# Kernel tuning notes

Hardware: AMD Instinct MI355X
Metric: run time of the kernel (lower is better)

## Reference

```python
import jax, jax.numpy as jnp
import numpy as np

B, NPB, K = 8, 4096, 16            # batches, points per batch, knn neighbors
IN_FEAT, OUT_FEAT, N_HEADS = 64, 64, 8
N = B * NPB
HD = OUT_FEAT // N_HEADS           # per-head dim (linear_w output width)
EPS = 1e-5


def _bn(x, g, b):
    # LayerNorm1d == BatchNorm1d over channel dim with stats across (N, k)
    m = jnp.mean(x, axis=(0, 1), keepdims=True)
    v = jnp.mean((x - m) ** 2, axis=(0, 1), keepdims=True)
    return (x - m) * jax.lax.rsqrt(v + EPS) * g + b


def _knn_idx(feat):
    # per-batch self-KNN in feature space (torch_geometric.nn.knn(x, x, k, batch, batch))
    f = feat.reshape(B, NPB, -1)
    sq = jnp.sum(f * f, axis=-1)                               # [B, n]
    d = sq[:, :, None] + sq[:, None, :] - 2.0 * jnp.einsum('bnc,bmc->bnm', f, f)
    _, idx = jax.lax.top_k(-d, K)                              # [B, n, K]
    idx = idx + (jnp.arange(B) * NPB)[:, None, None]           # global indices
    return idx.reshape(N, K)


def setup_inputs() -> dict:
    key = jax.random.key(0)
    ks = jax.random.split(key, 12)
    s = 0.05
    return {
        "p": jax.random.normal(ks[0], (N, 3), dtype=jnp.float32),
        "x": jax.random.normal(ks[1], (N, IN_FEAT), dtype=jnp.float32),
        "o": jnp.full((B,), NPB, dtype=jnp.int32),
        # q/k/v projections
        "wq": jax.random.normal(ks[2], (IN_FEAT, OUT_FEAT)) * s, "bq": jnp.zeros((OUT_FEAT,)),
        "wk": jax.random.normal(ks[3], (IN_FEAT, OUT_FEAT)) * s, "bk": jnp.zeros((OUT_FEAT,)),
        "wv": jax.random.normal(ks[4], (IN_FEAT, OUT_FEAT)) * s, "bv": jnp.zeros((OUT_FEAT,)),
        # linear_p: Linear(3,3) -> BN(3) -> ReLU -> Linear(3, out)
        "wp1": jax.random.normal(ks[5], (3, 3)) * s, "bp1": jnp.zeros((3,)),
        "gp": jnp.ones((3,)), "btp": jnp.zeros((3,)),
        "wp2": jax.random.normal(ks[6], (3, OUT_FEAT)) * s, "bp2": jnp.zeros((OUT_FEAT,)),
        # linear_w: BN(mid) -> ReLU -> Linear(mid, hd) -> BN(hd) -> ReLU -> Linear(hd, hd)
        "g1": jnp.ones((OUT_FEAT,)), "bt1": jnp.zeros((OUT_FEAT,)),
        "ww1": jax.random.normal(ks[7], (OUT_FEAT, HD)) * s, "bw1": jnp.zeros((HD,)),
        "g2": jnp.ones((HD,)), "bt2": jnp.zeros((HD,)),
        "ww2": jax.random.normal(ks[8], (HD, HD)) * s, "bw2": jnp.zeros((HD,)),
    }


def reference(p, x, o, wq, bq, wk, bk, wv, bv, wp1, bp1, gp, btp, wp2, bp2,
              g1, bt1, ww1, bw1, g2, bt2, ww2, bw2):
    # o encodes equal-size batches (NPB each); structure is baked into the knn helper.
    xq = x @ wq + bq                      # [N, mid]
    xk = x @ wk + bk                      # [N, mid]
    xv = x @ wv + bv                      # [N, out]
    idx_k = _knn_idx(xk)                  # KNN in k-feature space
    idx_v = _knn_idx(xv)                  # separate KNN in v-feature space (as in source)
    xk_g = xk[idx_k]                      # [N, K, mid]
    p_rel = p[idx_k] - p[:, None, :]      # grouped relative xyz [N, K, 3]
    xv_g = xv[idx_v]                      # [N, K, out]
    # position encoding MLP
    h = p_rel @ wp1 + bp1
    h = jax.nn.relu(_bn(h, gp, btp))
    p_r = h @ wp2 + bp2                   # [N, K, out]; einops.reduce with i=1 is identity
    # relation features and attention-weight MLP
    r = xk_g - xq[:, None, :] + p_r       # [N, K, mid]
    w = jax.nn.relu(_bn(r, g1, bt1)) @ ww1 + bw1
    w = jax.nn.relu(_bn(w, g2, bt2)) @ ww2 + bw2   # [N, K, HD]
    w = jax.nn.softmax(w, axis=1)         # softmax over neighbors
    comb = (xv_g + p_r).reshape(N, K, N_HEADS, HD)
    out = jnp.einsum('ntsi,nti->nsi', comb, w).reshape(N, OUT_FEAT)
    return out
```

## Files before the change

kernel.cpp:

```cpp
#include <hip/hip_runtime.h>
#include <hip/hip_bf16.h>

typedef __hip_bfloat16 bf16;

#define NPTS  32768
#define NPB   4096
#define NPAIR (NPTS*16)
#define IMASK 32767
#define EPSB  1e-5f

#define O_WQ  0
#define O_BQ  4096
#define O_WK  4160
#define O_BK  8256
#define O_WV  8320
#define O_BV  12416
#define O_WP1 12480
#define O_BP1 12489
#define O_GP  12492
#define O_BTP 12495
#define O_WP2 12498
#define O_BP2 12690
#define O_G1  12754
#define O_BT1 12818
#define O_WW1 12882
#define O_BW1 13394
#define O_G2  13402
#define O_BT2 13410
#define O_WW2 13418
#define O_BW2 13482
#define NPRM  13490

__device__ __forceinline__ float b2f(bf16 v){ return __bfloat162float(v); }
__device__ __forceinline__ float u16f(unsigned short u){ return __uint_as_float(((unsigned)u)<<16); }
__device__ __forceinline__ float ldany(const void* p, long long i, int f32){
    return f32 ? ((const float*)p)[i] : b2f(((const bf16*)p)[i]);
}

__device__ __forceinline__ void split2(float x, unsigned &h, unsigned &m){
    unsigned u  = __float_as_uint(x);
    unsigned hr = (u + 0x7FFFu + ((u>>16)&1u)) & 0xFFFF0000u;
    float xm = x - __uint_as_float(hr);
    h = hr >> 16;
    m = __float_as_uint(xm) >> 16;
}

__global__ __launch_bounds__(256) void k_sniff(const void* x, const void* wq, int* flags)
{
    __shared__ float red[2][4];
    const unsigned short* xu = (const unsigned short*)x;
    const unsigned short* wu = (const unsigned short*)wq;
    const int tid = threadIdx.x, lane = tid & 63, wvi = tid >> 6;
    float mx = fabsf(u16f(xu[tid]));
    float mw = fabsf(u16f(wu[tid]));
    for (int off = 32; off; off >>= 1){
        mx = fmaxf(mx, __shfl_down(mx, off));
        mw = fmaxf(mw, __shfl_down(mw, off));
    }
    if (lane == 0){ red[0][wvi] = mx; red[1][wvi] = mw; }
    __syncthreads();
    if (tid == 0){
        float ax = fmaxf(fmaxf(red[0][0], red[0][1]), fmaxf(red[0][2], red[0][3]));
        float aw = fmaxf(fmaxf(red[1][0], red[1][1]), fmaxf(red[1][2], red[1][3]));
        flags[0] = (ax > 1e6f) ? 1 : 0;
        flags[1] = (aw > 1e6f) ? 1 : 0;
    }
}

struct P20 { const void* p[20]; };

__global__ __launch_bounds__(256) void k_conv(P20 t, const void* __restrict__ p,
                                              const int* __restrict__ flags,
                                              float* __restrict__ prm, float* __restrict__ p32)
{
    const int i = blockIdx.x*256 + threadIdx.x;
    if (i < NPRM){
        const int f = flags[1];
        const int sz[20] = {4096,64,4096,64,4096,64,9,3,3,3,192,64,64,64,512,8,8,8,64,8};
        int seg = 0, rem = i;
        while (rem >= sz[seg]){ rem -= sz[seg]; ++seg; }
        prm[i] = ldany(t.p[seg], rem, f);
    } else {
        const int j = i - NPRM;
        if (j < NPTS*3) p32[j] = ldany(p, j, flags[0]);
    }
}

__global__ __launch_bounds__(256) void k_proj(
    const void* __restrict__ x, const int* __restrict__ flags,
    const float* __restrict__ prm,
    float* __restrict__ xq, float* __restrict__ xk, float* __restrict__ xv,
    float* __restrict__ sqk, float* __restrict__ sqv,
    unsigned* __restrict__ hkp, unsigned* __restrict__ mkp,
    unsigned* __restrict__ hvp, unsigned* __restrict__ mvp)
{
    __shared__ float WQ[4096], WK[4096], WV[4096], BQ[64], BK[64], BV[64];
    const int tid = threadIdx.x;
    for (int i = tid; i < 4096; i += 256){
        WQ[i] = prm[O_WQ+i]; WK[i] = prm[O_WK+i]; WV[i] = prm[O_WV+i];
    }
    if (tid < 64){ BQ[tid]=prm[O_BQ+tid]; BK[tid]=prm[O_BK+tid]; BV[tid]=prm[O_BV+tid]; }
    const int f32 = flags[0];
    __syncthreads();
    const int lane = tid & 63, wvi = tid >> 6;
    const int ptbase = blockIdx.x*16 + wvi*4;
    for (int it = 0; it < 4; ++it){
        const int pt = ptbase + it;
        float xl = ldany(x, (long long)pt*64 + lane, f32);
        float aq = BQ[lane], ak = BK[lane], av = BV[lane];
        #pragma unroll
        for (int k = 0; k < 64; ++k){
            float xb = __shfl(xl, k);
            aq += xb*WQ[k*64+lane];
            ak += xb*WK[k*64+lane];
            av += xb*WV[k*64+lane];
        }
        xq[pt*64+lane]=aq; xk[pt*64+lane]=ak; xv[pt*64+lane]=av;
        unsigned hk16, mk16, hv16, mv16;
        split2(ak, hk16, mk16); split2(av, hv16, mv16);
        unsigned hkn = __shfl_down(hk16,1), mkn = __shfl_down(mk16,1);
        unsigned hvn = __shfl_down(hv16,1), mvn = __shfl_down(mv16,1);
        if (!(lane & 1)){
            const int u = lane >> 3, pos = u ^ (pt & 7);
            const size_t gi = (size_t)pt*32 + pos*4 + ((lane & 7) >> 1);
            hkp[gi] = hk16 | (hkn<<16);  mkp[gi] = mk16 | (mkn<<16);
            hvp[gi] = hv16 | (hvn<<16);  mvp[gi] = mv16 | (mvn<<16);
        }
        float s1 = ak*ak, s2 = av*av;
        for (int off=32; off; off>>=1){ s1 += __shfl_down(s1,off); s2 += __shfl_down(s2,off); }
        if (lane==0){ sqk[pt]=s1; sqv[pt]=s2; }
    }
}


using bfrag  = __attribute__((ext_vector_type(8))) short;
using f32x4v = __attribute__((ext_vector_type(4))) float;

__device__ __forceinline__ int lds_sw(int row, int unit){
    return (row<<6) + (((unit ^ row) & 7)<<3);
}

__global__ __launch_bounds__(256, 4) void k_knn_part(
    const float* __restrict__ featk, const float* __restrict__ featv,
    const unsigned* __restrict__ hkp, const unsigned* __restrict__ mkp,
    const unsigned* __restrict__ hvp, const unsigned* __restrict__ mvp,
    const float* __restrict__ sqk, const float* __restrict__ sqv,
    const float* __restrict__ p32, const float* __restrict__ prm,
    int* __restrict__ idx_k, int* __restrict__ idx_v,
    float* __restrict__ part1)
{
    __shared__ __attribute__((aligned(16))) unsigned char smem[34048];
    __shared__ float bn1red[4][6];
    unsigned short* Ch = (unsigned short*)smem;
    unsigned short* Cm = (unsigned short*)(smem + 8192);
    float* Dt  = (float*)(smem + 16384);
    float* sqC = (float*)(smem + 16384 + 17408);
    unsigned long long* Lbuf = (unsigned long long*)smem;

    const int tid = threadIdx.x;
    const int swz = ((int)blockIdx.x & 7) * 128 + ((int)blockIdx.x >> 3);
    const int kid = swz >> 9;
    const int bid = swz & 511;
    const float*    feat = kid ? featv : featk;
    const float*    sq   = kid ? sqv  : sqk;
    const unsigned* hpl  = kid ? hvp : hkp;
    const unsigned* mpl  = kid ? mvp : mkp;
    const int b  = bid >> 6;
    const int qt = bid & 63;
    const int q0 = b*NPB + qt*64;
    const int cb = b*NPB;

    const int lane = tid & 63, wv = tid >> 6;
    const int lq = lane & 15, lg = lane >> 4;
    const int selq = (wv << 4) + (lane >> 2);
    const int sub  = lane & 3;
    const int owner = lane & ~3;
    const int row1 = tid >> 3, pos1 = tid & 7;
    const int row2 = row1 + 32;

    bfrag qh[2], qm[2];
    {
        const int qr = q0 + (wv<<4) + lq;
        #pragma unroll
        for (int ks = 0; ks < 2; ++ks){
            const int u0 = ks*4 + lg;
            const int pos = u0 ^ (qr & 7);
            union { uint4 u; bfrag v; } ch, cm;
            ch.u = *(const uint4*)&hpl[(size_t)qr*32 + pos*4];
            cm.u = *(const uint4*)&mpl[(size_t)qr*32 + pos*4];
            qh[ks] = ch.v; qm[ks] = cm.v;
        }
    }

    float d5[5]; int i5[5];
    #pragma unroll
    for (int i=0;i<5;++i){ d5[i] = 3.4e38f; i5[i] = 0; }

    const unsigned* hrow1 = hpl + (size_t)cb*32 + (size_t)row1*32 + pos1*4;
    const unsigned* hrow2 = hpl + (size_t)cb*32 + (size_t)row2*32 + pos1*4;
    const unsigned* mrow1 = mpl + (size_t)cb*32 + (size_t)row1*32 + pos1*4;
    const unsigned* mrow2 = mpl + (size_t)cb*32 + (size_t)row2*32 + pos1*4;
    const int ldsoff1 = row1*64 + pos1*8, ldsoff2 = row2*64 + pos1*8;

    {
        uint4 a1 = *(const uint4*)hrow1; uint4 a2 = *(const uint4*)hrow2;
        uint4 b1 = *(const uint4*)mrow1; uint4 b2 = *(const uint4*)mrow2;
        *(uint4*)&Ch[ldsoff1] = a1; *(uint4*)&Ch[ldsoff2] = a2;
        *(uint4*)&Cm[ldsoff1] = b1; *(uint4*)&Cm[ldsoff2] = b2;
        if (tid < 64) sqC[tid] = sq[cb + tid];
    }
    __syncthreads();

    #define MFMA_PHASE() { \
        _Pragma("unroll") \
        for (int ct = 0; ct < 4; ++ct){ \
            const int cd = ct*16 + lq; \
            union { uint4 u; bfrag v; } bh0u, bh1u, bm0u, bm1u; \
            bh0u.u = *(const uint4*)&Ch[lds_sw(cd, lg)]; \
            bh1u.u = *(const uint4*)&Ch[lds_sw(cd, 4+lg)]; \
            bm0u.u = *(const uint4*)&Cm[lds_sw(cd, lg)]; \
            bm1u.u = *(const uint4*)&Cm[lds_sw(cd, 4+lg)]; \
            f32x4v a = {0.f, 0.f, 0.f, 0.f}; \
            a = __builtin_amdgcn_mfma_f32_16x16x32_bf16(qm[0], bm0u.v, a, 0, 0, 0); \
            a = __builtin_amdgcn_mfma_f32_16x16x32_bf16(qm[1], bm1u.v, a, 0, 0, 0); \
            a = __builtin_amdgcn_mfma_f32_16x16x32_bf16(qh[0], bm0u.v, a, 0, 0, 0); \
            a = __builtin_amdgcn_mfma_f32_16x16x32_bf16(qm[0], bh0u.v, a, 0, 0, 0); \
            a = __builtin_amdgcn_mfma_f32_16x16x32_bf16(qh[1], bm1u.v, a, 0, 0, 0); \
            a = __builtin_amdgcn_mfma_f32_16x16x32_bf16(qm[1], bh1u.v, a, 0, 0, 0); \
            a = __builtin_amdgcn_mfma_f32_16x16x32_bf16(qh[0], bh0u.v, a, 0, 0, 0); \
            a = __builtin_amdgcn_mfma_f32_16x16x32_bf16(qh[1], bh1u.v, a, 0, 0, 0); \
            const float sc = sqC[ct*16 + lq]; \
            _Pragma("unroll") \
            for (int r = 0; r < 4; ++r) \
                Dt[((wv<<4) + (lg<<2) + r)*68 + ct*16 + lq] = sc - 2.f*a[r]; \
        } }

    MFMA_PHASE()

    for (int chn = 0; chn < 64; ++chn){
        __syncthreads();
        const bool more = (chn+1 < 64);
        uint4 a1, a2, b1, b2; float sqr = 0.f;
        if (more){
            const size_t co = (size_t)(chn+1)*2048;
            a1 = *(const uint4*)(hrow1 + co); a2 = *(const uint4*)(hrow2 + co);
            b1 = *(const uint4*)(mrow1 + co); b2 = *(const uint4*)(mrow2 + co);
            if (tid < 64) sqr = sq[cb + (chn+1)*64 + tid];
        }
        {
            float worst = __shfl(d5[4], owner+3);
            unsigned m16 = 0;
            const int rowoff = selq*68 + sub*16;
            #pragma unroll
            for (int r = 0; r < 4; ++r){
                float4 v = *(const float4*)&Dt[rowoff + 4*r];
                m16 |= (v.x < worst ? 1u : 0u) << (4*r+0);
                m16 |= (v.y < worst ? 1u : 0u) << (4*r+1);
                m16 |= (v.z < worst ? 1u : 0u) << (4*r+2);
                m16 |= (v.w < worst ? 1u : 0u) << (4*r+3);
            }
            unsigned ma = __shfl(m16, owner+0), mb = __shfl(m16, owner+1);
            unsigned mc = __shfl(m16, owner+2), md = __shfl(m16, owner+3);
            unsigned long long m = (unsigned long long)ma
                                 | ((unsigned long long)mb << 16)
                                 | ((unsigned long long)mc << 32)
                                 | ((unsigned long long)md << 48);
            const int qrow = selq*68;
            const int c0 = cb + chn*64;
            const int prevlane = (lane - 1) & 63;
            while (m){
                int c = (int)__builtin_ctzll(m); m &= m - 1;
                float d = Dt[qrow + c];
                int gi = c0 + c;
                float pl = __shfl(d5[4], prevlane);
                int   pi = __shfl(i5[4], prevlane);
                bool takePrev = (sub != 0) && (pl > d);
                float v  = takePrev ? pl : d;
                int   vi = takePrev ? pi : gi;
                #pragma unroll
                for (int i = 4; i >= 1; --i){
                    bool sh   = d5[i-1] > v;
                    bool here = !sh && (d5[i] > v);
                    d5[i] = sh ? d5[i-1] : (here ? v  : d5[i]);
                    i5[i] = sh ? i5[i-1] : (here ? vi : i5[i]);
                }
                bool h0 = d5[0] > v;
                d5[0] = h0 ? v  : d5[0];
                i5[0] = h0 ? vi : i5[0];
            }
        }
        if (more){
            *(uint4*)&Ch[ldsoff1] = a1; *(uint4*)&Ch[ldsoff2] = a2;
            *(uint4*)&Cm[ldsoff1] = b1; *(uint4*)&Cm[ldsoff2] = b2;
            if (tid < 64) sqC[tid] = sqr;
        }
        __syncthreads();
        if (more) MFMA_PHASE()
    }
    #undef MFMA_PHASE

    unsigned long long k5[5];
    {
        const float* qrow = feat + (size_t)(q0 + selq)*64;
        #pragma unroll
        for (int s = 0; s < 5; ++s){
            const int gi = i5[s];
            const float* crow = feat + (size_t)gi*64;
            float acc = 0.f;
            #pragma unroll
            for (int k4 = 0; k4 < 16; ++k4){
                float4 qv = *(const float4*)&qrow[4*k4];
                float4 cv = *(const float4*)&crow[4*k4];
                acc += qv.x*cv.x; acc += qv.y*cv.y; acc += qv.z*cv.z; acc += qv.w*cv.w;
            }
            float d = sq[gi] - 2.f*acc;
            unsigned ud = __float_as_uint(d);
            ud ^= (ud & 0x80000000u) ? 0xFFFFFFFFu : 0x80000000u;
            k5[s] = ((unsigned long long)ud << 32) | (unsigned)gi;
        }
    }
    #pragma unroll
    for (int pass = 0; pass < 5; ++pass){
        #pragma unroll
        for (int i = (pass & 1); i + 1 < 5; i += 2){
            unsigned long long a = k5[i], bb = k5[i+1];
            bool sw = a > bb;
            k5[i]   = sw ? bb : a;
            k5[i+1] = sw ? a : bb;
        }
    }
    __syncthreads();
    #pragma unroll
    for (int j = 0; j < 5; ++j) Lbuf[(size_t)tid*6 + j] = k5[j];
    Lbuf[(size_t)tid*6 + 5] = ~0ull;
    __syncthreads();
    int fi[16];
    #pragma unroll
    for (int i = 0; i < 16; ++i) fi[i] = 0;
    if (sub == 0){
        const unsigned long long* L0 = &Lbuf[(size_t)(tid+0)*6];
        const unsigned long long* L1 = &Lbuf[(size_t)(tid+1)*6];
        const unsigned long long* L2 = &Lbuf[(size_t)(tid+2)*6];
        const unsigned long long* L3 = &Lbuf[(size_t)(tid+3)*6];
        int p0 = 0, p1 = 0, p2 = 0, p3 = 0;
        #pragma unroll
        for (int o = 0; o < 16; ++o){
            unsigned long long b0 = L0[p0], b1v = L1[p1], b2v = L2[p2], b3v = L3[p3];
            unsigned long long m01 = (b0  < b1v) ? b0  : b1v;  int s01 = (b0  < b1v) ? 0 : 1;
            unsigned long long m23 = (b2v < b3v) ? b2v : b3v;  int s23 = (b2v < b3v) ? 2 : 3;
            unsigned long long mm  = (m01 < m23) ? m01 : m23;  int ss  = (m01 < m23) ? s01 : s23;
            fi[o] = (int)(unsigned)(mm & 0xFFFFFFFFull);
            if      (ss == 0) ++p0;
            else if (ss == 1) ++p1;
            else if (ss == 2) ++p2;
            else              ++p3;
        }
        int* idx_out = kid ? idx_v : idx_k;
        #pragma unroll
        for (int i4 = 0; i4 < 4; ++i4)
            *(int4*)&idx_out[(size_t)(q0+selq)*16 + 4*i4] =
                make_int4(fi[4*i4], fi[4*i4+1], fi[4*i4+2], fi[4*i4+3]);
    }

    if (kid == 0){
        const float w00=prm[O_WP1+0], w01=prm[O_WP1+1], w02=prm[O_WP1+2];
        const float w10=prm[O_WP1+3], w11=prm[O_WP1+4], w12=prm[O_WP1+5];
        const float w20=prm[O_WP1+6], w21=prm[O_WP1+7], w22=prm[O_WP1+8];
        const float bb0=prm[O_BP1+0], bb1=prm[O_BP1+1], bb2=prm[O_BP1+2];
        const size_t gq = (size_t)(q0 + selq);
        const float px=p32[gq*3+0], py=p32[gq*3+1], pz=p32[gq*3+2];
        float s0=0.f,s1=0.f,s2=0.f,t0=0.f,t1=0.f,t2=0.f;
        #pragma unroll
        for (int o = 0; o < 16; ++o){
            int gi = __shfl(fi[o], owner);
            if ((o & 3) == sub){
                const int j = gi & IMASK;
                float rx = p32[j*3+0]-px, ry = p32[j*3+1]-py, rz = p32[j*3+2]-pz;
                float h0 = bb0 + rx*w00 + ry*w10 + rz*w20;
                float h1 = bb1 + rx*w01 + ry*w11 + rz*w21;
                float h2 = bb2 + rx*w02 + ry*w12 + rz*w22;
                s0+=h0; s1+=h1; s2+=h2; t0+=h0*h0; t1+=h1*h1; t2+=h2*h2;
            }
        }
        #pragma unroll
        for (int off = 1; off < 64; off <<= 1){
            s0+=__shfl_down(s0,off); s1+=__shfl_down(s1,off); s2+=__shfl_down(s2,off);
            t0+=__shfl_down(t0,off); t1+=__shfl_down(t1,off); t2+=__shfl_down(t2,off);
        }
        if (lane == 0){
            bn1red[wv][0]=s0; bn1red[wv][1]=s1; bn1red[wv][2]=s2;
            bn1red[wv][3]=t0; bn1red[wv][4]=t1; bn1red[wv][5]=t2;
        }
        __syncthreads();
        if (tid < 6)
            part1[(size_t)tid*512 + bid] =
                bn1red[0][tid]+bn1red[1][tid]+bn1red[2][tid]+bn1red[3][tid];
    }
}

__global__ __launch_bounds__(256) void k_bnred_par(
    const float* __restrict__ part, int G, int C,
    const float* __restrict__ gamma, const float* __restrict__ beta,
    float* __restrict__ aff, float invCount)
{
    __shared__ float rs[4], rq[4];
    const int c = blockIdx.x;
    const int tid = threadIdx.x;
    float s = 0.f, q = 0.f;
    for (int g = tid; g < G; g += 256){
        s += part[(size_t)c*G + g];
        q += part[(size_t)(C+c)*G + g];
    }
    for (int off=32; off; off>>=1){ s += __shfl_down(s,off); q += __shfl_down(q,off); }
    if ((tid & 63) == 0){ rs[tid>>6] = s; rq[tid>>6] = q; }
    __syncthreads();
    if (tid == 0){
        float S = rs[0]+rs[1]+rs[2]+rs[3], Q = rq[0]+rq[1]+rq[2]+rq[3];
        float mean = S*invCount;
        float var  = fmaxf(Q*invCount - mean*mean, 0.f);
        float sc = gamma[c] * rsqrtf(var + EPSB);
        aff[c]   = sc;
        aff[C+c] = beta[c] - mean*sc;
    }
}

__global__ __launch_bounds__(256) void k_rstats(
    const float* __restrict__ p32,
    const float* __restrict__ xq, const float* __restrict__ xk, const int* __restrict__ idx_k,
    const float* __restrict__ bn1aff, const float* __restrict__ prm,
    float* __restrict__ part2)
{
    const int tid = threadIdx.x, lane = tid & 63, wvi = tid >> 6;
    const float wa = prm[O_WP2+lane], wb = prm[O_WP2+64+lane], wc = prm[O_WP2+128+lane];
    const float bpc = prm[O_BP2+lane];
    const float w00=prm[O_WP1+0], w01=prm[O_WP1+1], w02=prm[O_WP1+2];
    const float w10=prm[O_WP1+3], w11=prm[O_WP1+4], w12=prm[O_WP1+5];
    const float w20=prm[O_WP1+6], w21=prm[O_WP1+7], w22=prm[O_WP1+8];
    const float bb0=prm[O_BP1+0], bb1=prm[O_BP1+1], bb2=prm[O_BP1+2];
    const float sc0=bn1aff[0], sc1=bn1aff[1], sc2=bn1aff[2];
    const float sh0=bn1aff[3], sh1=bn1aff[4], sh2=bn1aff[5];
    const int base = (blockIdx.x*4 + wvi) * 64;
    float asum=0.f, asq=0.f;
    float px=0.f, py=0.f, pz=0.f, xql=0.f;
    for (int e4 = 0; e4 < 16; ++e4){
        const int gb = base + e4*4;
        if ((gb & 15) == 0){
            const int n = gb >> 4;
            px=p32[n*3+0]; py=p32[n*3+1]; pz=p32[n*3+2];
            xql = xq[(size_t)n*64+lane];
        }
        int4 jj = *(const int4*)&idx_k[gb];
        int j[4] = { jj.x & IMASK, jj.y & IMASK, jj.z & IMASK, jj.w & IMASK };
        float kx[4], qx[4][3];
        #pragma unroll
        for (int u=0;u<4;++u){
            qx[u][0]=p32[j[u]*3+0]; qx[u][1]=p32[j[u]*3+1]; qx[u][2]=p32[j[u]*3+2];
            kx[u] = xk[(size_t)j[u]*64+lane];
        }
        #pragma unroll
        for (int u=0;u<4;++u){
            float rx = qx[u][0]-px, ry = qx[u][1]-py, rz = qx[u][2]-pz;
            float h0 = bb0 + rx*w00 + ry*w10 + rz*w20;
            float h1 = bb1 + rx*w01 + ry*w11 + rz*w21;
            float h2 = bb2 + rx*w02 + ry*w12 + rz*w22;
            float r0 = fmaxf(h0*sc0+sh0, 0.f), r1 = fmaxf(h1*sc1+sh1,0.f), r2 = fmaxf(h2*sc2+sh2,0.f);
            float pr = r0*wa + r1*wb + r2*wc + bpc;
            float rv = kx[u] - xql + pr;
            asum += rv; asq += rv*rv;
        }
    }
    __shared__ float red[4][128];
    red[wvi][lane] = asum; red[wvi][64+lane] = asq;
    __syncthreads();
    if (tid < 128)
        part2[(size_t)tid*2048 + blockIdx.x] = red[0][tid]+red[1][tid]+red[2][tid]+red[3][tid];
}

__global__ __launch_bounds__(256) void k_wstats(
    const float* __restrict__ p32,
    const float* __restrict__ xq, const float* __restrict__ xk, const int* __restrict__ idx_k,
    const float* __restrict__ bn1aff, const float* __restrict__ prm,
    const float* __restrict__ bn2aff, float* __restrict__ wbuf, float* __restrict__ part3)
{
    __shared__ float4 PRW[64];
    __shared__ float2 SS2[64];
    __shared__ float4 W1A[64], W1B[64];
    const int tid = threadIdx.x;
    if (tid < 64){
        PRW[tid] = make_float4(prm[O_WP2+tid], prm[O_WP2+64+tid], prm[O_WP2+128+tid], prm[O_BP2+tid]);
        SS2[tid] = make_float2(bn2aff[tid], bn2aff[64+tid]);
        W1A[tid] = make_float4(prm[O_WW1+tid*8+0],prm[O_WW1+tid*8+1],prm[O_WW1+tid*8+2],prm[O_WW1+tid*8+3]);
        W1B[tid] = make_float4(prm[O_WW1+tid*8+4],prm[O_WW1+tid*8+5],prm[O_WW1+tid*8+6],prm[O_WW1+tid*8+7]);
    }
    __syncthreads();
    const int g = blockIdx.x*256 + tid;
    const int n = g >> 4;
    const int j = idx_k[g] & IMASK;
    const float w00=prm[O_WP1+0], w01=prm[O_WP1+1], w02=prm[O_WP1+2];
    const float w10=prm[O_WP1+3], w11=prm[O_WP1+4], w12=prm[O_WP1+5];
    const float w20=prm[O_WP1+6], w21=prm[O_WP1+7], w22=prm[O_WP1+8];
    const float bb0=prm[O_BP1+0], bb1=prm[O_BP1+1], bb2=prm[O_BP1+2];
    const float sc0=bn1aff[0], sc1=bn1aff[1], sc2=bn1aff[2];
    const float sh0=bn1aff[3], sh1=bn1aff[4], sh2=bn1aff[5];
    float rx = p32[j*3+0] - p32[n*3+0];
    float ry = p32[j*3+1] - p32[n*3+1];
    float rz = p32[j*3+2] - p32[n*3+2];
    float h0 = bb0 + rx*w00 + ry*w10 + rz*w20;
    float h1 = bb1 + rx*w01 + ry*w11 + rz*w21;
    float h2 = bb2 + rx*w02 + ry*w12 + rz*w22;
    float r0 = fmaxf(h0*sc0+sh0, 0.f), r1 = fmaxf(h1*sc1+sh1,0.f), r2 = fmaxf(h2*sc2+sh2,0.f);
    float wacc[8];
    #pragma unroll
    for (int i=0;i<8;++i) wacc[i] = prm[O_BW1+i];
    const float4* kr = (const float4*)(xk + (size_t)j*64);
    const float4* qr = (const float4*)(xq + (size_t)n*64);
    #pragma unroll
    for (int c4=0;c4<16;++c4){
        float4 kv = kr[c4], qv = qr[c4];
        float kvv[4] = {kv.x,kv.y,kv.z,kv.w};
        float qvv[4] = {qv.x,qv.y,qv.z,qv.w};
        #pragma unroll
        for (int d=0; d<4; ++d){
            int c = 4*c4 + d;
            float4 pw = PRW[c]; float2 ss = SS2[c];
            float pr = r0*pw.x + r1*pw.y + r2*pw.z + pw.w;
            float rr = kvv[d] - qvv[d] + pr;
            float y = fmaxf(rr*ss.x + ss.y, 0.f);
            float4 wA = W1A[c], wB = W1B[c];
            wacc[0]+=y*wA.x; wacc[1]+=y*wA.y; wacc[2]+=y*wA.z; wacc[3]+=y*wA.w;
            wacc[4]+=y*wB.x; wacc[5]+=y*wB.y; wacc[6]+=y*wB.z; wacc[7]+=y*wB.w;
        }
    }
    *(float4*)&wbuf[(size_t)g*8]   = make_float4(wacc[0],wacc[1],wacc[2],wacc[3]);
    *(float4*)&wbuf[(size_t)g*8+4] = make_float4(wacc[4],wacc[5],wacc[6],wacc[7]);
    float st[16];
    #pragma unroll
    for (int i=0;i<8;++i){ st[i]=wacc[i]; st[8+i]=wacc[i]*wacc[i]; }
    for (int off=32; off; off>>=1){
        #pragma unroll
        for (int k=0;k<16;++k) st[k] += __shfl_down(st[k], off);
    }
    __shared__ float red[4][16];
    const int lane = tid&63, wvi = tid>>6;
    if (lane==0){
        #pragma unroll
        for (int k=0;k<16;++k) red[wvi][k]=st[k];
    }
    __syncthreads();
    if (tid < 16)
        part3[(size_t)tid*2048 + blockIdx.x] = red[0][tid]+red[1][tid]+red[2][tid]+red[3][tid];
}

__global__ __launch_bounds__(256) void k_out(
    const float* __restrict__ p32, const float* __restrict__ xv,
    const int* __restrict__ idx_k, const int* __restrict__ idx_v,
    const float* __restrict__ bn1aff, const float* __restrict__ prm,
    const float* __restrict__ wbuf, const float* __restrict__ bn3aff,
    const int* __restrict__ flags, void* __restrict__ out)
{
    const int tid = threadIdx.x, lane = tid & 63, wvi = tid >> 6;
    const int n = blockIdx.x*4 + wvi;
    const int f32 = flags[0];
    const float w00=prm[O_WP1+0], w01=prm[O_WP1+1], w02=prm[O_WP1+2];
    const float w10=prm[O_WP1+3], w11=prm[O_WP1+4], w12=prm[O_WP1+5];
    const float w20=prm[O_WP1+6], w21=prm[O_WP1+7], w22=prm[O_WP1+8];
    const float bb0=prm[O_BP1+0], bb1=prm[O_BP1+1], bb2=prm[O_BP1+2];
    const float sc0=bn1aff[0], sc1=bn1aff[1], sc2=bn1aff[2];
    const float sh0=bn1aff[3], sh1=bn1aff[4], sh2=bn1aff[5];
    const float wa=prm[O_WP2+lane], wb=prm[O_WP2+64+lane], wc=prm[O_WP2+128+lane];
    const float bpc=prm[O_BP2+lane];
    const int i = lane & 7;
    float s3[8], t3[8], w2col[8];
    #pragma unroll
    for (int m=0;m<8;++m){
        s3[m]=bn3aff[m]; t3[m]=bn3aff[8+m];
        w2col[m]=prm[O_WW2+m*8+i];
    }
    const float bw2i = prm[O_BW2+i];
    const float px=p32[n*3+0], py=p32[n*3+1], pz=p32[n*3+2];
    float comb[16], wf[16];
    #pragma unroll
    for (int t=0;t<16;++t){
        const int g = n*16 + t;
        const int jk = idx_k[g] & IMASK;
        const int jv = idx_v[g] & IMASK;
        float rx=p32[jk*3+0]-px, ry=p32[jk*3+1]-py, rz=p32[jk*3+2]-pz;
        float h0=bb0+rx*w00+ry*w10+rz*w20;
        float h1=bb1+rx*w01+ry*w11+rz*w21;
        float h2=bb2+rx*w02+ry*w12+rz*w22;
        float r0=fmaxf(h0*sc0+sh0,0.f), r1=fmaxf(h1*sc1+sh1,0.f), r2=fmaxf(h2*sc2+sh2,0.f);
        float pr=r0*wa+r1*wb+r2*wc+bpc;
        float4 wA = *(const float4*)&wbuf[(size_t)g*8];
        float4 wB = *(const float4*)&wbuf[(size_t)g*8+4];
        float wm[8] = {wA.x,wA.y,wA.z,wA.w,wB.x,wB.y,wB.z,wB.w};
        float acc = bw2i;
        #pragma unroll
        for (int m=0;m<8;++m){
            float y3 = fmaxf(wm[m]*s3[m]+t3[m],0.f);
            acc += y3*w2col[m];
        }
        wf[t]=acc;
        comb[t]=xv[(size_t)jv*64+lane]+pr;
    }
    float mx = wf[0];
    #pragma unroll
    for (int t=1;t<16;++t) mx = fmaxf(mx, wf[t]);
    float ssum=0.f, osum=0.f;
    #pragma unroll
    for (int t=0;t<16;++t){ float e = __expf(wf[t]-mx); ssum += e; osum += e*comb[t]; }
    const float v = osum / ssum;
    if (f32) ((float*)out)[(size_t)n*64+lane] = v;
    else     ((bf16*)out)[(size_t)n*64+lane] = __float2bfloat16(v);
}

extern "C" void kernel_launch(void* const* d_in, const int* in_sizes, int n_in,
                              void* d_out, int out_size, void* d_ws, size_t ws_size,
                              hipStream_t stream)
{
    const void* p  = d_in[0];
    const void* x  = d_in[1];
    P20 prms;
    for (int i = 0; i < 20; ++i) prms.p[i] = d_in[3+i];

    float* W = (float*)d_ws;
    float* xqf    = W + 0;
    float* xkf    = W + 2097152;
    float* xvf    = W + 4194304;
    float* sqk    = W + 6291456;
    float* sqv    = W + 6324224;
    int*   idx_k  = (int*)(W + 6356992);
    int*   idx_v  = (int*)(W + 6881280);
    float* p32    = W + 7405568;
    float* prm    = W + 7503872;
    float* part1  = W + 7517376;
    float* part2  = W + 7529664;
    float* part3  = W + 7791808;
    float* bn1aff = W + 7824576;
    float* bn2aff = W + 7824592;
    float* bn3aff = W + 7824720;
    int*   flags  = (int*)(W + 7824736);
    unsigned* hkp = (unsigned*)(W + 7824752);
    unsigned* mkp = (unsigned*)(W + 7824752 + 1048576);
    unsigned* hvp = (unsigned*)(W + 7824752 + 2097152);
    unsigned* mvp = (unsigned*)(W + 7824752 + 3145728);
    float* wbuf   = W + 7824752;

    const float invP = 1.f / (float)NPAIR;

    k_sniff<<<1,256,0,stream>>>(x, d_in[3], flags);
    k_conv<<<(NPRM + NPTS*3 + 255)/256,256,0,stream>>>(prms, p, flags, prm, p32);
    k_proj<<<2048,256,0,stream>>>(x, flags, prm, xqf,xkf,xvf, sqk,sqv, hkp,mkp,hvp,mvp);
    k_knn_part<<<1024,256,0,stream>>>(xkf, xvf, hkp,mkp,hvp,mvp, sqk, sqv,
                                      p32, prm, idx_k, idx_v, part1);
    k_bnred_par<<<3,256,0,stream>>>(part1, 512, 3, prm+O_GP, prm+O_BTP, bn1aff, invP);
    k_rstats<<<2048,256,0,stream>>>(p32, xqf, xkf, idx_k, bn1aff, prm, part2);
    k_bnred_par<<<64,256,0,stream>>>(part2, 2048, 64, prm+O_G1, prm+O_BT1, bn2aff, invP);
    k_wstats<<<2048,256,0,stream>>>(p32, xqf, xkf, idx_k, bn1aff, prm, bn2aff, wbuf, part3);
    k_bnred_par<<<8,256,0,stream>>>(part3, 2048, 8, prm+O_G2, prm+O_BT2, bn3aff, invP);
    k_out<<<8192,256,0,stream>>>(p32, xvf, idx_k, idx_v, bn1aff, prm,
                                 wbuf, bn3aff, flags, d_out);
}
```

Baseline: 609.5 us.

## Merge sniff into conv, register-resident projection weights, async global-to-LDS KNN staging

Folds the dtype-sniff kernel into the conversion kernel, with every block recomputing the flags locally, which removes one launch. The projection kernel now gives each wave a single weight matrix held in registers instead of staging all three in LDS. The KNN candidate tiles are now loaded with direct global-to-LDS loads, issued right after the MFMA phase so they overlap the top-k selection, replacing the register round-trip copy. The risks are higher register pressure in k_proj and the correctness of the global_load_lds layout against the swizzled LDS indexing.

```diff
diff --git a/kernel.cpp b/kernel.cpp
--- a/kernel.cpp
+++ b/kernel.cpp
@@ -45,11 +45,25 @@
     m = __float_as_uint(xm) >> 16;
 }
 
-__global__ __launch_bounds__(256) void k_sniff(const void* x, const void* wq, int* flags)
+__device__ __forceinline__ void gll16(const void* g, void* l){
+    __builtin_amdgcn_global_load_lds((const __attribute__((address_space(1))) unsigned*)(g),
+                                     (__attribute__((address_space(3))) unsigned*)(l), 16, 0, 0);
+}
+__device__ __forceinline__ void gll4(const void* g, void* l){
+    __builtin_amdgcn_global_load_lds((const __attribute__((address_space(1))) unsigned*)(g),
+                                     (__attribute__((address_space(3))) unsigned*)(l), 4, 0, 0);
+}
+
+struct P20 { const void* p[20]; };
+
+__global__ __launch_bounds__(256) void k_conv(P20 t, const void* __restrict__ p,
+                                              const void* __restrict__ x, const void* __restrict__ wq0,
+                                              float* __restrict__ prm, float* __restrict__ p32,
+                                              int* __restrict__ flags)
 {
     __shared__ float red[2][4];
     const unsigned short* xu = (const unsigned short*)x;
-    const unsigned short* wu = (const unsigned short*)wq;
+    const unsigned short* wu = (const unsigned short*)wq0;
     const int tid = threadIdx.x, lane = tid & 63, wvi = tid >> 6;
     float mx = fabsf(u16f(xu[tid]));
     float mw = fabsf(u16f(wu[tid]));
@@ -59,34 +73,24 @@
     }
     if (lane == 0){ red[0][wvi] = mx; red[1][wvi] = mw; }
     __syncthreads();
-    if (tid == 0){
-        float ax = fmaxf(fmaxf(red[0][0], red[0][1]), fmaxf(red[0][2], red[0][3]));
-        float aw = fmaxf(fmaxf(red[1][0], red[1][1]), fmaxf(red[1][2], red[1][3]));
-        flags[0] = (ax > 1e6f) ? 1 : 0;
-        flags[1] = (aw > 1e6f) ? 1 : 0;
-    }
-}
-
-struct P20 { const void* p[20]; };
-
-__global__ __launch_bounds__(256) void k_conv(P20 t, const void* __restrict__ p,
-                                              const int* __restrict__ flags,
-                                              float* __restrict__ prm, float* __restrict__ p32)
-{
-    const int i = blockIdx.x*256 + threadIdx.x;
+    const float ax = fmaxf(fmaxf(red[0][0], red[0][1]), fmaxf(red[0][2], red[0][3]));
+    const float aw = fmaxf(fmaxf(red[1][0], red[1][1]), fmaxf(red[1][2], red[1][3]));
+    const int f0 = (ax > 1e6f) ? 1 : 0;
+    const int f1 = (aw > 1e6f) ? 1 : 0;
+    if (blockIdx.x == 0 && tid == 0){ flags[0] = f0; flags[1] = f1; }
+    const int i = blockIdx.x*256 + tid;
     if (i < NPRM){
-        const int f = flags[1];
         const int sz[20] = {4096,64,4096,64,4096,64,9,3,3,3,192,64,64,64,512,8,8,8,64,8};
         int seg = 0, rem = i;
         while (rem >= sz[seg]){ rem -= sz[seg]; ++seg; }
-        prm[i] = ldany(t.p[seg], rem, f);
+        prm[i] = ldany(t.p[seg], rem, f1);
     } else {
         const int j = i - NPRM;
-        if (j < NPTS*3) p32[j] = ldany(p, j, flags[0]);
-    }
-}
-
-__global__ __launch_bounds__(256) void k_proj(
+        if (j < NPTS*3) p32[j] = ldany(p, j, f0);
+    }
+}
+
+__global__ __launch_bounds__(192) void k_proj(
     const void* __restrict__ x, const int* __restrict__ flags,
     const float* __restrict__ prm,
     float* __restrict__ xq, float* __restrict__ xk, float* __restrict__ xv,
@@ -94,41 +98,36 @@
     unsigned* __restrict__ hkp, unsigned* __restrict__ mkp,
     unsigned* __restrict__ hvp, unsigned* __restrict__ mvp)
 {
-    __shared__ float WQ[4096], WK[4096], WV[4096], BQ[64], BK[64], BV[64];
-    const int tid = threadIdx.x;
-    for (int i = tid; i < 4096; i += 256){
-        WQ[i] = prm[O_WQ+i]; WK[i] = prm[O_WK+i]; WV[i] = prm[O_WV+i];
-    }
-    if (tid < 64){ BQ[tid]=prm[O_BQ+tid]; BK[tid]=prm[O_BK+tid]; BV[tid]=prm[O_BV+tid]; }
+    const int tid = threadIdx.x, lane = tid & 63, wvi = tid >> 6;
     const int f32 = flags[0];
-    __syncthreads();
-    const int lane = tid & 63, wvi = tid >> 6;
-    const int ptbase = blockIdx.x*16 + wvi*4;
-    for (int it = 0; it < 4; ++it){
+    const int OW = (wvi==0) ? O_WQ : (wvi==1) ? O_WK : O_WV;
+    const int OB = (wvi==0) ? O_BQ : (wvi==1) ? O_BK : O_BV;
+    float Wc[64];
+    #pragma unroll
+    for (int k = 0; k < 64; ++k) Wc[k] = prm[OW + k*64 + lane];
+    const float bias = prm[OB + lane];
+    float* outp = (wvi==0) ? xq : (wvi==1) ? xk : xv;
+    const int ptbase = blockIdx.x*32;
+    for (int it = 0; it < 32; ++it){
         const int pt = ptbase + it;
         float xl = ldany(x, (long long)pt*64 + lane, f32);
-        float aq = BQ[lane], ak = BK[lane], av = BV[lane];
-        #pragma unroll
-        for (int k = 0; k < 64; ++k){
-            float xb = __shfl(xl, k);
-            aq += xb*WQ[k*64+lane];
-            ak += xb*WK[k*64+lane];
-            av += xb*WV[k*64+lane];
-        }
-        xq[pt*64+lane]=aq; xk[pt*64+lane]=ak; xv[pt*64+lane]=av;
-        unsigned hk16, mk16, hv16, mv16;
-        split2(ak, hk16, mk16); split2(av, hv16, mv16);
-        unsigned hkn = __shfl_down(hk16,1), mkn = __shfl_down(mk16,1);
-        unsigned hvn = __shfl_down(hv16,1), mvn = __shfl_down(mv16,1);
-        if (!(lane & 1)){
-            const int u = lane >> 3, pos = u ^ (pt & 7);
-            const size_t gi = (size_t)pt*32 + pos*4 + ((lane & 7) >> 1);
-            hkp[gi] = hk16 | (hkn<<16);  mkp[gi] = mk16 | (mkn<<16);
-            hvp[gi] = hv16 | (hvn<<16);  mvp[gi] = mv16 | (mvn<<16);
-        }
-        float s1 = ak*ak, s2 = av*av;
-        for (int off=32; off; off>>=1){ s1 += __shfl_down(s1,off); s2 += __shfl_down(s2,off); }
-        if (lane==0){ sqk[pt]=s1; sqv[pt]=s2; }
+        float acc = bias;
+        #pragma unroll
+        for (int k = 0; k < 64; ++k) acc += __shfl(xl, k)*Wc[k];
+        outp[(size_t)pt*64 + lane] = acc;
+        if (wvi){
+            unsigned h16, m16; split2(acc, h16, m16);
+            unsigned hn = __shfl_down(h16,1), mn = __shfl_down(m16,1);
+            if (!(lane & 1)){
+                const int u = lane >> 3, pos = u ^ (pt & 7);
+                const size_t gi = (size_t)pt*32 + pos*4 + ((lane & 7) >> 1);
+                if (wvi == 1){ hkp[gi] = h16 | (hn<<16);  mkp[gi] = m16 | (mn<<16); }
+                else         { hvp[gi] = h16 | (hn<<16);  mvp[gi] = m16 | (mn<<16); }
+            }
+            float s = acc*acc;
+            for (int off=32; off; off>>=1) s += __shfl_down(s, off);
+            if (lane == 0){ if (wvi == 1) sqk[pt] = s; else sqv[pt] = s; }
+        }
     }
 }
 
@@ -175,8 +174,6 @@
     const int selq = (wv << 4) + (lane >> 2);
     const int sub  = lane & 3;
     const int owner = lane & ~3;
-    const int row1 = tid >> 3, pos1 = tid & 7;
-    const int row2 = row1 + 32;
 
     bfrag qh[2], qm[2];
     {
@@ -196,20 +193,17 @@
     #pragma unroll
     for (int i=0;i<5;++i){ d5[i] = 3.4e38f; i5[i] = 0; }
 
-    const unsigned* hrow1 = hpl + (size_t)cb*32 + (size_t)row1*32 + pos1*4;
-    const unsigned* hrow2 = hpl + (size_t)cb*32 + (size_t)row2*32 + pos1*4;
-    const unsigned* mrow1 = mpl + (size_t)cb*32 + (size_t)row1*32 + pos1*4;
-    const unsigned* mrow2 = mpl + (size_t)cb*32 + (size_t)row2*32 + pos1*4;
-    const int ldsoff1 = row1*64 + pos1*8, ldsoff2 = row2*64 + pos1*8;
-
-    {
-        uint4 a1 = *(const uint4*)hrow1; uint4 a2 = *(const uint4*)hrow2;
-        uint4 b1 = *(const uint4*)mrow1; uint4 b2 = *(const uint4*)mrow2;
-        *(uint4*)&Ch[ldsoff1] = a1; *(uint4*)&Ch[ldsoff2] = a2;
-        *(uint4*)&Cm[ldsoff1] = b1; *(uint4*)&Cm[ldsoff2] = b2;
-        if (tid < 64) sqC[tid] = sq[cb + tid];
-    }
-    __syncthreads();
+    const unsigned* hrowA = hpl + (size_t)cb*32 + (size_t)tid*4;
+    const unsigned* mrowA = mpl + (size_t)cb*32 + (size_t)tid*4;
+
+    #define STAGE(CHN) { \
+        const size_t co = (size_t)(CHN)*2048; \
+        gll16(hrowA + co,        (void*)&Ch[8*tid]); \
+        gll16(hrowA + co + 1024, (void*)&Ch[8*tid + 2048]); \
+        gll16(mrowA + co,        (void*)&Cm[8*tid]); \
+        gll16(mrowA + co + 1024, (void*)&Cm[8*tid + 2048]); \
+        if (tid < 64) gll4(sq + cb + (CHN)*64 + tid, (void*)&sqC[tid]); \
+    }
 
     #define MFMA_PHASE() { \
         _Pragma("unroll") \
@@ -235,18 +229,13 @@
                 Dt[((wv<<4) + (lg<<2) + r)*68 + ct*16 + lq] = sc - 2.f*a[r]; \
         } }
 
-    MFMA_PHASE()
+    STAGE(0)
+    __syncthreads();
 
     for (int chn = 0; chn < 64; ++chn){
+        MFMA_PHASE()
         __syncthreads();
-        const bool more = (chn+1 < 64);
-        uint4 a1, a2, b1, b2; float sqr = 0.f;
-        if (more){
-            const size_t co = (size_t)(chn+1)*2048;
-            a1 = *(const uint4*)(hrow1 + co); a2 = *(const uint4*)(hrow2 + co);
-            b1 = *(const uint4*)(mrow1 + co); b2 = *(const uint4*)(mrow2 + co);
-            if (tid < 64) sqr = sq[cb + (chn+1)*64 + tid];
-        }
+        if (chn + 1 < 64) STAGE(chn+1)
         {
             float worst = __shfl(d5[4], owner+3);
             unsigned m16 = 0;
@@ -289,15 +278,10 @@
                 i5[0] = h0 ? vi : i5[0];
             }
         }
-        if (more){
-            *(uint4*)&Ch[ldsoff1] = a1; *(uint4*)&Ch[ldsoff2] = a2;
-            *(uint4*)&Cm[ldsoff1] = b1; *(uint4*)&Cm[ldsoff2] = b2;
-            if (tid < 64) sqC[tid] = sqr;
-        }
         __syncthreads();
-        if (more) MFMA_PHASE()
     }
     #undef MFMA_PHASE
+    #undef STAGE
 
     unsigned long long k5[5];
     {
@@ -647,9 +631,8 @@
 
     const float invP = 1.f / (float)NPAIR;
 
-    k_sniff<<<1,256,0,stream>>>(x, d_in[3], flags);
-    k_conv<<<(NPRM + NPTS*3 + 255)/256,256,0,stream>>>(prms, p, flags, prm, p32);
-    k_proj<<<2048,256,0,stream>>>(x, flags, prm, xqf,xkf,xvf, sqk,sqv, hkp,mkp,hvp,mvp);
+    k_conv<<<(NPRM + NPTS*3 + 255)/256,256,0,stream>>>(prms, p, x, d_in[3], prm, p32, flags);
+    k_proj<<<1024,192,0,stream>>>(x, flags, prm, xqf,xkf,xvf, sqk,sqv, hkp,mkp,hvp,mvp);
     k_knn_part<<<1024,256,0,stream>>>(xkf, xvf, hkp,mkp,hvp,mvp, sqk, sqv,
                                       p32, prm, idx_k, idx_v, part1);
     k_bnred_par<<<3,256,0,stream>>>(part1, 512, 3, prm+O_GP, prm+O_BTP, bn1aff, invP);
```

After: 614.0 us. About the same (+0.7%).
